# Performance work log

Hardware: AMD Instinct MI355X
Metric: run time of the kernel (lower is better)

The kernel has to match this reference:

```python
import jax, jax.numpy as jnp
import numpy as np

B, S, D, H = 4, 2048, 1024, 16
HD = D // H  # head_dim = 64


def setup_inputs() -> dict:
    key = jax.random.key(0)
    ks = jax.random.split(key, 10)
    scale = 1.0 / np.sqrt(D)
    x = jax.random.normal(ks[0], (B, S, D), dtype=jnp.float32)
    mask = jax.random.randint(ks[1], (B, S, S), 0, 2, dtype=jnp.int32)
    Wq = jax.random.normal(ks[2], (D, D), dtype=jnp.float32) * scale
    Wk = jax.random.normal(ks[3], (D, D), dtype=jnp.float32) * scale
    Wv = jax.random.normal(ks[4], (D, D), dtype=jnp.float32) * scale
    Wo = jax.random.normal(ks[5], (D, D), dtype=jnp.float32) * scale
    bq = jax.random.normal(ks[6], (D,), dtype=jnp.float32) * 0.01
    bk = jax.random.normal(ks[7], (D,), dtype=jnp.float32) * 0.01
    bv = jax.random.normal(ks[8], (D,), dtype=jnp.float32) * 0.01
    bo = jax.random.normal(ks[9], (D,), dtype=jnp.float32) * 0.01
    return {"x": x, "mask": mask, "Wq": Wq, "bq": bq, "Wk": Wk, "bk": bk,
            "Wv": Wv, "bv": bv, "Wo": Wo, "bo": bo}


def reference(x, mask, Wq, bq, Wk, bk, Wv, bv, Wo, bo):
    # QKV projections (nn.Linear: x @ W^T + b; W stored pre-transposed here as [D,D])
    q = x @ Wq + bq  # [B,S,D]
    k = x @ Wk + bk
    v = x @ Wv + bv
    # split heads -> [B,H,S,HD]
    def heads(t):
        return t.reshape(B, S, H, HD).transpose(0, 2, 1, 3)
    q, k, v = heads(q), heads(k), heads(v)
    scores = jnp.einsum('bhqd,bhkd->bhqk', q, k) / jnp.sqrt(jnp.float32(HD))
    # mask: [B,S,S] -> broadcast over heads; positions where mask==0 get -inf
    scores = jnp.where(mask[:, None, :, :] == 0, -jnp.inf, scores)
    attn = jax.nn.softmax(scores, axis=-1)
    attn = jnp.where(jnp.isnan(attn), 0.0, attn)  # nan_to_num(nan=0.0)
    out = jnp.einsum('bhqk,bhkd->bhqd', attn, v)  # [B,H,S,HD]
    out = out.transpose(0, 2, 1, 3).reshape(B, S, D)
    return out @ Wo + bo
```

## Files before the change

kernel.cpp:

```cpp
#include <hip/hip_runtime.h>
#include <hip/hip_bf16.h>
#include <stdint.h>

#define B_  4
#define S_  2048
#define D_  1024
#define H_  16
#define HD_ 64

typedef __attribute__((ext_vector_type(4))) float f32x4;
typedef __attribute__((ext_vector_type(8))) short bf16x8;

typedef const unsigned int __attribute__((address_space(1)))* gas_ptr;
typedef unsigned int __attribute__((address_space(3)))* las_ptr;

__device__ __forceinline__ void async16(const void* g, void* l) {
  __builtin_amdgcn_global_load_lds((gas_ptr)g, (las_ptr)l, 16, 0, 0);
}

__global__ __launch_bounds__(256) void cvt_x(const float* __restrict__ in,
                                             __hip_bfloat16* __restrict__ out,
                                             int n) {
  const int i = (blockIdx.x * blockDim.x + threadIdx.x) * 4;
  if (i >= n) return;
  const float4 v = *(const float4*)(in + i);
  union { ushort4 u; __hip_bfloat16 h[4]; } o;
  o.h[0] = (__hip_bfloat16)v.x;
  o.h[1] = (__hip_bfloat16)v.y;
  o.h[2] = (__hip_bfloat16)v.z;
  o.h[3] = (__hip_bfloat16)v.w;
  *(ushort4*)(out + i) = o.u;
}

__global__ __launch_bounds__(256) void expand_mask(const int* __restrict__ mk,
                                                   uint2* __restrict__ xm) {
  const unsigned j = blockIdx.x * 256 + threadIdx.x;
  const int mt = j & 3, quad = (j >> 2) & 3, kt = (j >> 4) & 31;
  const int q = (j >> 9) & 2047, b = j >> 20;
  const size_t row = (size_t)b * 2048 + q;
  const int key = kt * 64 + mt * 16 + quad * 4;
  const int4 m = *(const int4*)(mk + row * 2048 + key);
  uint2 o;
  o.x = (m.x ? 0xFFFFu : 0u) | (m.y ? 0xFFFF0000u : 0u);
  o.y = (m.z ? 0xFFFFu : 0u) | (m.w ? 0xFFFF0000u : 0u);
  xm[j] = o;
}

__global__ void transpose_w(const float* __restrict__ Wq,
                            const float* __restrict__ Wk,
                            const float* __restrict__ Wv,
                            const float* __restrict__ Wo,
                            __hip_bfloat16* __restrict__ Wt_qkv,
                            __hip_bfloat16* __restrict__ Wt_o) {
  __shared__ float t[32][33];
  const int z = blockIdx.z;
  const float* W = (z == 0) ? Wq : (z == 1) ? Wk : (z == 2) ? Wv : Wo;
  __hip_bfloat16* Wt = (z < 3) ? (Wt_qkv + (size_t)z * D_ * D_) : Wt_o;
  const int x = blockIdx.x * 32 + threadIdx.x;
  const int y = blockIdx.y * 32 + threadIdx.y;
  t[threadIdx.y][threadIdx.x] = W[(size_t)y * D_ + x];
  __syncthreads();
  const int xo = blockIdx.y * 32 + threadIdx.x;
  const int yo = blockIdx.x * 32 + threadIdx.y;
  Wt[(size_t)yo * D_ + xo] = (__hip_bfloat16)t[threadIdx.x][threadIdx.y];
}

__global__ __launch_bounds__(256) void gemm_qkv(
    const __hip_bfloat16* __restrict__ A,
    const __hip_bfloat16* __restrict__ Bt,
    const float* __restrict__ bq,
    const float* __restrict__ bk,
    const float* __restrict__ bv,
    __hip_bfloat16* __restrict__ QKo,
    __hip_bfloat16* __restrict__ Vt) {
  __shared__ __hip_bfloat16 sA[128 * 32];
  __shared__ __hip_bfloat16 sB[128 * 32];
  const int K = 1024;
  const int tid  = threadIdx.x;
  const int wave = tid >> 6;
  const int lane = tid & 63;
  const int quad = lane >> 4;
  const int l16  = lane & 15;
  const int wg  = blockIdx.x;
  const int swz = (wg & 7) * 192 + (wg >> 3);
  const int bm = (swz / 24) * 128;
  const int bn = (swz % 24) * 128;
  const int wm = (wave >> 1) * 64;
  const int wn = (wave & 1) * 64;

  const int r0 = wave * 2, r1 = wave * 2 + 1;
  const int lrow = lane >> 2;
  const int lcol = (lane & 3) * 8;

  const __hip_bfloat16* ga0 = A  + (size_t)(bm + r0 * 16 + lrow) * K + lcol;
  const __hip_bfloat16* ga1 = A  + (size_t)(bm + r1 * 16 + lrow) * K + lcol;
  const __hip_bfloat16* gb0 = Bt + (size_t)(bn + r0 * 16 + lrow) * K + lcol;
  const __hip_bfloat16* gb1 = Bt + (size_t)(bn + r1 * 16 + lrow) * K + lcol;
  char* la0 = (char*)sA + r0 * 1024;
  char* la1 = (char*)sA + r1 * 1024;
  char* lb0 = (char*)sB + r0 * 1024;
  char* lb1 = (char*)sB + r1 * 1024;

  const char* pa = (const char*)sA + (wm + l16) * 64 + quad * 16;
  const char* pb = (const char*)sB + (wn + l16) * 64 + quad * 16;

  f32x4 acc[4][4] = {};

  for (int k0 = 0; k0 < K; k0 += 32) {
    async16(ga0 + k0, la0);
    async16(ga1 + k0, la1);
    async16(gb0 + k0, lb0);
    async16(gb1 + k0, lb1);
    __syncthreads();
    bf16x8 af[4], bf[4];
#pragma unroll
    for (int mt = 0; mt < 4; ++mt) af[mt] = *(const bf16x8*)(pa + mt * 1024);
#pragma unroll
    for (int nt = 0; nt < 4; ++nt) bf[nt] = *(const bf16x8*)(pb + nt * 1024);
#pragma unroll
    for (int mt = 0; mt < 4; ++mt)
#pragma unroll
      for (int nt = 0; nt < 4; ++nt)
        acc[mt][nt] = __builtin_amdgcn_mfma_f32_16x16x32_bf16(af[mt], bf[nt], acc[mt][nt], 0, 0, 0);
    __syncthreads();
  }

#pragma unroll
  for (int mt = 0; mt < 4; ++mt) {
    const int row = bm + wm + mt * 16 + quad * 4;
#pragma unroll
    for (int nt = 0; nt < 4; ++nt) {
      const int col = bn + wn + nt * 16 + l16;
      f32x4 v = acc[mt][nt];
      if (col < 2048) {
        const float bias = (col < 1024) ? bq[col] : bk[col - 1024];
        const float sc = (col < 1024) ? 0.18033688011f : 1.0f;
#pragma unroll
        for (int r = 0; r < 4; ++r)
          QKo[(size_t)(row + r) * 2048 + col] = (__hip_bfloat16)((v[r] + bias) * sc);
      } else {
        const int cv = col - 2048;
        const float bias = bv[cv];
        const int hh = cv >> 6, d = cv & 63;
        const int bb = row >> 11, s0 = row & 2047;
        union { __hip_bfloat16 h[4]; unsigned long long u; } pk;
#pragma unroll
        for (int r = 0; r < 4; ++r) pk.h[r] = (__hip_bfloat16)(v[r] + bias);
        *(unsigned long long*)(Vt + ((size_t)(bb * 16 + hh) * 64 + d) * 2048 + s0) = pk.u;
      }
    }
  }
}

__global__ __launch_bounds__(256) void gemm_out(
    const __hip_bfloat16* __restrict__ A,
    const __hip_bfloat16* __restrict__ Bt,
    const float* __restrict__ b0,
    float* __restrict__ C,
    int N, int K) {
  __shared__ __hip_bfloat16 sA[128 * 32];
  __shared__ __hip_bfloat16 sB[128 * 32];
  const int tid  = threadIdx.x;
  const int wave = tid >> 6;
  const int lane = tid & 63;
  const int quad = lane >> 4;
  const int l16  = lane & 15;
  const int wg  = blockIdx.x;
  const int swz = (wg & 7) * 64 + (wg >> 3);
  const int bm = (swz >> 3) * 128;
  const int bn = (swz & 7) * 128;
  const int wm = (wave >> 1) * 64;
  const int wn = (wave & 1) * 64;

  const int r0 = wave * 2, r1 = wave * 2 + 1;
  const int lrow = lane >> 2;
  const int lcol = (lane & 3) * 8;

  const __hip_bfloat16* ga0 = A  + (size_t)(bm + r0 * 16 + lrow) * K + lcol;
  const __hip_bfloat16* ga1 = A  + (size_t)(bm + r1 * 16 + lrow) * K + lcol;
  const __hip_bfloat16* gb0 = Bt + (size_t)(bn + r0 * 16 + lrow) * K + lcol;
  const __hip_bfloat16* gb1 = Bt + (size_t)(bn + r1 * 16 + lrow) * K + lcol;
  char* la0 = (char*)sA + r0 * 1024;
  char* la1 = (char*)sA + r1 * 1024;
  char* lb0 = (char*)sB + r0 * 1024;
  char* lb1 = (char*)sB + r1 * 1024;

  const char* pa = (const char*)sA + (wm + l16) * 64 + quad * 16;
  const char* pb = (const char*)sB + (wn + l16) * 64 + quad * 16;

  f32x4 acc[4][4] = {};

  for (int k0 = 0; k0 < K; k0 += 32) {
    async16(ga0 + k0, la0);
    async16(ga1 + k0, la1);
    async16(gb0 + k0, lb0);
    async16(gb1 + k0, lb1);
    __syncthreads();
    bf16x8 af[4], bf[4];
#pragma unroll
    for (int mt = 0; mt < 4; ++mt) af[mt] = *(const bf16x8*)(pa + mt * 1024);
#pragma unroll
    for (int nt = 0; nt < 4; ++nt) bf[nt] = *(const bf16x8*)(pb + nt * 1024);
#pragma unroll
    for (int mt = 0; mt < 4; ++mt)
#pragma unroll
      for (int nt = 0; nt < 4; ++nt)
        acc[mt][nt] = __builtin_amdgcn_mfma_f32_16x16x32_bf16(af[mt], bf[nt], acc[mt][nt], 0, 0, 0);
    __syncthreads();
  }

#pragma unroll
  for (int mt = 0; mt < 4; ++mt) {
    const int row = bm + wm + mt * 16 + quad * 4;
#pragma unroll
    for (int nt = 0; nt < 4; ++nt) {
      const int col = bn + wn + nt * 16 + l16;
      const float bias = b0[col];
      f32x4 v = acc[mt][nt];
#pragma unroll
      for (int r = 0; r < 4; ++r)
        C[(size_t)(row + r) * N + col] = v[r] + bias;
    }
  }
}

__global__ __launch_bounds__(256, 4) void flash_attn(
    const __hip_bfloat16* __restrict__ QK,
    const __hip_bfloat16* __restrict__ Vt,
    const uint4* __restrict__ XM,
    __hip_bfloat16* __restrict__ O) {
  __shared__ __hip_bfloat16 sK[2][64 * 64];
  __shared__ __hip_bfloat16 sV[2][64 * 64];

  const int qt = blockIdx.x, h = blockIdx.y, b = blockIdx.z;
  const int tid = threadIdx.x;
  const int wave = tid >> 6, lane = tid & 63, quad = lane >> 4, l16 = lane & 15;
  const int qbase = qt * 128;
  const size_t brow = (size_t)b * S_;
  const int bh = b * H_ + h;

  bf16x8 qf[2][2];
#pragma unroll
  for (int g = 0; g < 2; ++g) {
    const __hip_bfloat16* qrow =
        QK + (brow + qbase + g * 64 + wave * 16 + l16) * 2048 + h * 64;
#pragma unroll
    for (int c = 0; c < 2; ++c)
      qf[g][c] = *(const bf16x8*)(qrow + c * 32 + quad * 8);
  }

  const int srow = lane >> 3;
  const int schk = (lane & 7) ^ srow;
  const __hip_bfloat16* gk0 =
      QK + (brow + wave * 16 + srow) * 2048 + 1024 + h * 64 + schk * 8;
  const __hip_bfloat16* gk1 = gk0 + (size_t)8 * 2048;
  const __hip_bfloat16* gv0 =
      Vt + ((size_t)bh * 64 + wave * 16 + srow) * 2048 + schk * 8;
  const __hip_bfloat16* gv1 = gv0 + (size_t)8 * 2048;
  char* const lK[2] = {(char*)&sK[0][0] + wave * 2048, (char*)&sK[1][0] + wave * 2048};
  char* const lV[2] = {(char*)&sV[0][0] + wave * 2048, (char*)&sV[1][0] + wave * 2048};

  const uint4* xpa = XM + ((brow + qbase + wave * 16 + l16) * 256 + quad * 2);
  const uint4* xpb = xpa + (size_t)64 * 256;

  const int xl = l16 & 7;
  const int koff0 = ((quad ^ xl) * 16);
  const int rowb = l16 * 128;

  const bf16x8 onesv = {(short)0x3F80, (short)0x3F80, (short)0x3F80, (short)0x3F80,
                        (short)0x3F80, (short)0x3F80, (short)0x3F80, (short)0x3F80};
  f32x4 lacc[2] = {};
  f32x4 oacc[2][4] = {};

  async16(gk0, lK[0]);
  async16(gk1, lK[0] + 1024);
  async16(gv0, lV[0]);
  async16(gv1, lV[0] + 1024);
  uint4 x0a = xpa[0], x1a = xpa[1], x0b = xpb[0], x1b = xpb[1];
  gk0 += (size_t)64 * 2048; gk1 += (size_t)64 * 2048;
  gv0 += 64; gv1 += 64;
  __syncthreads();

  const int NT = S_ / 64;
  for (int kt = 0; kt < NT; ++kt) {
    const int cur = kt & 1, nxt = cur ^ 1;

    if (kt + 1 < NT) {
      async16(gk0, lK[nxt]);
      async16(gk1, lK[nxt] + 1024);
      async16(gv0, lV[nxt]);
      async16(gv1, lV[nxt] + 1024);
      gk0 += (size_t)64 * 2048; gk1 += (size_t)64 * 2048;
      gv0 += 64; gv1 += 64;
    }
    const uint4 ca0 = x0a, ca1 = x1a, cb0 = x0b, cb1 = x1b;
    const int kn = (kt + 1 < NT) ? kt + 1 : kt;
    x0a = xpa[kn * 8]; x1a = xpa[kn * 8 + 1];
    x0b = xpb[kn * 8]; x1b = xpb[kn * 8 + 1];

    const char* bK = (const char*)&sK[cur][0] + rowb;
    unsigned pl[2][4][2];
#pragma unroll
    for (int mt = 0; mt < 4; ++mt) {
      const bf16x8 kf0 = *(const bf16x8*)(bK + mt * 2048 + koff0);
      const bf16x8 kf1 = *(const bf16x8*)(bK + mt * 2048 + (koff0 ^ 64));
      f32x4 a0 = {}, a1 = {};
      __builtin_amdgcn_s_setprio(1);
      a0 = __builtin_amdgcn_mfma_f32_16x16x32_bf16(kf0, qf[0][0], a0, 0, 0, 0);
      a0 = __builtin_amdgcn_mfma_f32_16x16x32_bf16(kf1, qf[0][1], a0, 0, 0, 0);
      a1 = __builtin_amdgcn_mfma_f32_16x16x32_bf16(kf0, qf[1][0], a1, 0, 0, 0);
      a1 = __builtin_amdgcn_mfma_f32_16x16x32_bf16(kf1, qf[1][1], a1, 0, 0, 0);
      __builtin_amdgcn_s_setprio(0);
#pragma unroll
      for (int g = 0; g < 2; ++g) {
        const uint4 cc = g ? ((mt < 2) ? cb0 : cb1) : ((mt < 2) ? ca0 : ca1);
        const unsigned w0 = (mt & 1) ? cc.z : cc.x;
        const unsigned w1 = (mt & 1) ? cc.w : cc.y;
        const f32x4 av = g ? a1 : a0;
        union { __hip_bfloat16 h[2]; unsigned u; } c0, c1;
        c0.h[0] = (__hip_bfloat16)__builtin_amdgcn_exp2f(av[0]);
        c0.h[1] = (__hip_bfloat16)__builtin_amdgcn_exp2f(av[1]);
        c1.h[0] = (__hip_bfloat16)__builtin_amdgcn_exp2f(av[2]);
        c1.h[1] = (__hip_bfloat16)__builtin_amdgcn_exp2f(av[3]);
        pl[g][mt][0] = c0.u & w0;
        pl[g][mt][1] = c1.u & w1;
      }
    }

    bf16x8 pf[2][2];
#pragma unroll
    for (int g = 0; g < 2; ++g)
#pragma unroll
      for (int c = 0; c < 2; ++c) {
        unsigned e0 = pl[g][2 * c][0], o0 = pl[g][2 * c + 1][0];
        unsigned e1 = pl[g][2 * c][1], o1 = pl[g][2 * c + 1][1];
        asm("v_permlane32_swap_b32 %0, %1" : "+v"(e0), "+v"(o0));
        asm("v_permlane16_swap_b32 %0, %1" : "+v"(e0), "+v"(o0));
        asm("v_permlane32_swap_b32 %0, %1" : "+v"(e1), "+v"(o1));
        asm("v_permlane16_swap_b32 %0, %1" : "+v"(e1), "+v"(o1));
        union { unsigned u[4]; bf16x8 v; } uu;
        uu.u[0] = e0; uu.u[1] = e1; uu.u[2] = o0; uu.u[3] = o1;
        pf[g][c] = uu.v;
      }

    const char* bV = (const char*)&sV[cur][0] + rowb;
    __builtin_amdgcn_s_setprio(1);
#pragma unroll
    for (int ht = 0; ht < 4; ++ht) {
      const bf16x8 vf0 = *(const bf16x8*)(bV + ht * 2048 + koff0);
      const bf16x8 vf1 = *(const bf16x8*)(bV + ht * 2048 + (koff0 ^ 64));
      oacc[0][ht] = __builtin_amdgcn_mfma_f32_16x16x32_bf16(vf0, pf[0][0], oacc[0][ht], 0, 0, 0);
      oacc[0][ht] = __builtin_amdgcn_mfma_f32_16x16x32_bf16(vf1, pf[0][1], oacc[0][ht], 0, 0, 0);
      oacc[1][ht] = __builtin_amdgcn_mfma_f32_16x16x32_bf16(vf0, pf[1][0], oacc[1][ht], 0, 0, 0);
      oacc[1][ht] = __builtin_amdgcn_mfma_f32_16x16x32_bf16(vf1, pf[1][1], oacc[1][ht], 0, 0, 0);
    }
    lacc[0] = __builtin_amdgcn_mfma_f32_16x16x32_bf16(onesv, pf[0][0], lacc[0], 0, 0, 0);
    lacc[0] = __builtin_amdgcn_mfma_f32_16x16x32_bf16(onesv, pf[0][1], lacc[0], 0, 0, 0);
    lacc[1] = __builtin_amdgcn_mfma_f32_16x16x32_bf16(onesv, pf[1][0], lacc[1], 0, 0, 0);
    lacc[1] = __builtin_amdgcn_mfma_f32_16x16x32_bf16(onesv, pf[1][1], lacc[1], 0, 0, 0);
    __builtin_amdgcn_s_setprio(0);

    __syncthreads();
  }

#pragma unroll
  for (int g = 0; g < 2; ++g) {
    const float l = lacc[g][0];
    const float inv = (l > 0.f) ? 1.f / l : 0.f;
    __hip_bfloat16* orow =
        O + (brow + qbase + g * 64 + wave * 16 + l16) * 1024 + h * 64;
#pragma unroll
    for (int ht = 0; ht < 4; ++ht) {
      union { __hip_bfloat16 h[4]; unsigned long long u; } ok_;
#pragma unroll
      for (int r = 0; r < 4; ++r) ok_.h[r] = (__hip_bfloat16)(oacc[g][ht][r] * inv);
      *(unsigned long long*)(orow + ht * 16 + quad * 4) = ok_.u;
    }
  }
}

extern "C" void kernel_launch(void* const* d_in, const int* in_sizes, int n_in,
                              void* d_out, int out_size, void* d_ws, size_t ws_size,
                              hipStream_t stream) {
  const float* x  = (const float*)d_in[0];
  const int*   mk = (const int*)d_in[1];
  const float* Wq = (const float*)d_in[2];
  const float* bq = (const float*)d_in[3];
  const float* Wk = (const float*)d_in[4];
  const float* bk = (const float*)d_in[5];
  const float* Wv = (const float*)d_in[6];
  const float* bv = (const float*)d_in[7];
  const float* Wo = (const float*)d_in[8];
  const float* bo = (const float*)d_in[9];
  float* out = (float*)d_out;

  __hip_bfloat16* X16    = (__hip_bfloat16*)d_ws;
  __hip_bfloat16* Wt_qkv = X16 + (size_t)B_ * S_ * D_;
  __hip_bfloat16* Wt_o   = Wt_qkv + (size_t)3 * D_ * D_;
  __hip_bfloat16* QK     = Wt_o + (size_t)D_ * D_;
  __hip_bfloat16* Vt     = QK + (size_t)B_ * S_ * 2 * D_;
  __hip_bfloat16* Obuf   = Vt + (size_t)B_ * H_ * HD_ * S_;
  unsigned* xmask = (unsigned*)(Obuf + (size_t)B_ * S_ * D_);

  const int nx = B_ * S_ * D_;
  cvt_x<<<dim3((nx / 4 + 255) / 256), 256, 0, stream>>>(x, X16, nx);
  transpose_w<<<dim3(32, 32, 4), dim3(32, 32), 0, stream>>>(Wq, Wk, Wv, Wo, Wt_qkv, Wt_o);
  expand_mask<<<dim3((int)((size_t)B_ * S_ * S_ / 4 / 256)), 256, 0, stream>>>(
      mk, (uint2*)xmask);
  gemm_qkv<<<dim3(24 * 64), 256, 0, stream>>>(
      X16, Wt_qkv, bq, bk, bv, QK, Vt);
  flash_attn<<<dim3(S_ / 128, H_, B_), 256, 0, stream>>>(
      QK, Vt, (const uint4*)xmask, Obuf);
  gemm_out<<<dim3(8 * 64), 256, 0, stream>>>(
      Obuf, Wt_o, bo, out, D_, D_);
}
```

Measured before the change: 360.2 us.

## Double GEMM K-tile to 64 with XOR-swizzled LDS layout in projection kernels

Both projection GEMMs now stage 128x64 bf16 tiles of A and B per iteration instead of 128x32. That halves the number of __syncthreads barriers and loop iterations over K. The LDS layout is XOR-swizzled on 16-byte chunks, on both the global_load_lds writes and the fragment reads, to avoid bank conflicts on the wider 128-byte rows. LDS use per block doubles to 32KB, which may reduce occupancy, and loads are still not overlapped with compute.

```diff
diff --git a/kernel.cpp b/kernel.cpp
--- a/kernel.cpp
+++ b/kernel.cpp
@@ -73,8 +73,8 @@
     const float* __restrict__ bv,
     __hip_bfloat16* __restrict__ QKo,
     __hip_bfloat16* __restrict__ Vt) {
-  __shared__ __hip_bfloat16 sA[128 * 32];
-  __shared__ __hip_bfloat16 sB[128 * 32];
+  __shared__ __hip_bfloat16 sA[128 * 64];
+  __shared__ __hip_bfloat16 sB[128 * 64];
   const int K = 1024;
   const int tid  = threadIdx.x;
   const int wave = tid >> 6;
@@ -88,40 +88,41 @@
   const int wm = (wave >> 1) * 64;
   const int wn = (wave & 1) * 64;
 
-  const int r0 = wave * 2, r1 = wave * 2 + 1;
-  const int lrow = lane >> 2;
-  const int lcol = (lane & 3) * 8;
-
-  const __hip_bfloat16* ga0 = A  + (size_t)(bm + r0 * 16 + lrow) * K + lcol;
-  const __hip_bfloat16* ga1 = A  + (size_t)(bm + r1 * 16 + lrow) * K + lcol;
-  const __hip_bfloat16* gb0 = Bt + (size_t)(bn + r0 * 16 + lrow) * K + lcol;
-  const __hip_bfloat16* gb1 = Bt + (size_t)(bn + r1 * 16 + lrow) * K + lcol;
-  char* la0 = (char*)sA + r0 * 1024;
-  char* la1 = (char*)sA + r1 * 1024;
-  char* lb0 = (char*)sB + r0 * 1024;
-  char* lb1 = (char*)sB + r1 * 1024;
-
-  const char* pa = (const char*)sA + (wm + l16) * 64 + quad * 16;
-  const char* pb = (const char*)sB + (wn + l16) * 64 + quad * 16;
+  const int srow = lane >> 3;
+  const int schk = (lane & 7) ^ srow;
+  const __hip_bfloat16* gA = A  + (size_t)(bm + wave * 32 + srow) * K + schk * 8;
+  const __hip_bfloat16* gB = Bt + (size_t)(bn + wave * 32 + srow) * K + schk * 8;
+  char* const lA = (char*)sA + wave * 32 * 128;
+  char* const lB = (char*)sB + wave * 32 * 128;
+
+  const int xl = l16 & 7;
+  const int koff = (quad ^ xl) * 16;
+  const char* pa = (const char*)sA + (wm + l16) * 128;
+  const char* pb = (const char*)sB + (wn + l16) * 128;
 
   f32x4 acc[4][4] = {};
 
-  for (int k0 = 0; k0 < K; k0 += 32) {
-    async16(ga0 + k0, la0);
-    async16(ga1 + k0, la1);
-    async16(gb0 + k0, lb0);
-    async16(gb1 + k0, lb1);
+  for (int k0 = 0; k0 < K; k0 += 64) {
+#pragma unroll
+    for (int t = 0; t < 4; ++t) {
+      async16(gA + (size_t)(t * 8) * K + k0, lA + t * 1024);
+      async16(gB + (size_t)(t * 8) * K + k0, lB + t * 1024);
+    }
     __syncthreads();
-    bf16x8 af[4], bf[4];
-#pragma unroll
-    for (int mt = 0; mt < 4; ++mt) af[mt] = *(const bf16x8*)(pa + mt * 1024);
-#pragma unroll
-    for (int nt = 0; nt < 4; ++nt) bf[nt] = *(const bf16x8*)(pb + nt * 1024);
-#pragma unroll
-    for (int mt = 0; mt < 4; ++mt)
-#pragma unroll
-      for (int nt = 0; nt < 4; ++nt)
-        acc[mt][nt] = __builtin_amdgcn_mfma_f32_16x16x32_bf16(af[mt], bf[nt], acc[mt][nt], 0, 0, 0);
+#pragma unroll
+    for (int c = 0; c < 2; ++c) {
+      const int off = koff ^ (c * 64);
+      bf16x8 af[4], bf[4];
+#pragma unroll
+      for (int mt = 0; mt < 4; ++mt) af[mt] = *(const bf16x8*)(pa + mt * 2048 + off);
+#pragma unroll
+      for (int nt = 0; nt < 4; ++nt) bf[nt] = *(const bf16x8*)(pb + nt * 2048 + off);
+#pragma unroll
+      for (int mt = 0; mt < 4; ++mt)
+#pragma unroll
+        for (int nt = 0; nt < 4; ++nt)
+          acc[mt][nt] = __builtin_amdgcn_mfma_f32_16x16x32_bf16(af[mt], bf[nt], acc[mt][nt], 0, 0, 0);
+    }
     __syncthreads();
   }
 
@@ -158,8 +159,8 @@
     const float* __restrict__ b0,
     float* __restrict__ C,
     int N, int K) {
-  __shared__ __hip_bfloat16 sA[128 * 32];
-  __shared__ __hip_bfloat16 sB[128 * 32];
+  __shared__ __hip_bfloat16 sA[128 * 64];
+  __shared__ __hip_bfloat16 sB[128 * 64];
   const int tid  = threadIdx.x;
   const int wave = tid >> 6;
   const int lane = tid & 63;
@@ -172,40 +173,41 @@
   const int wm = (wave >> 1) * 64;
   const int wn = (wave & 1) * 64;
 
-  const int r0 = wave * 2, r1 = wave * 2 + 1;
-  const int lrow = lane >> 2;
-  const int lcol = (lane & 3) * 8;
-
-  const __hip_bfloat16* ga0 = A  + (size_t)(bm + r0 * 16 + lrow) * K + lcol;
-  const __hip_bfloat16* ga1 = A  + (size_t)(bm + r1 * 16 + lrow) * K + lcol;
-  const __hip_bfloat16* gb0 = Bt + (size_t)(bn + r0 * 16 + lrow) * K + lcol;
-  const __hip_bfloat16* gb1 = Bt + (size_t)(bn + r1 * 16 + lrow) * K + lcol;
-  char* la0 = (char*)sA + r0 * 1024;
-  char* la1 = (char*)sA + r1 * 1024;
-  char* lb0 = (char*)sB + r0 * 1024;
-  char* lb1 = (char*)sB + r1 * 1024;
-
-  const char* pa = (const char*)sA + (wm + l16) * 64 + quad * 16;
-  const char* pb = (const char*)sB + (wn + l16) * 64 + quad * 16;
+  const int srow = lane >> 3;
+  const int schk = (lane & 7) ^ srow;
+  const __hip_bfloat16* gA = A  + (size_t)(bm + wave * 32 + srow) * K + schk * 8;
+  const __hip_bfloat16* gB = Bt + (size_t)(bn + wave * 32 + srow) * K + schk * 8;
+  char* const lA = (char*)sA + wave * 32 * 128;
+  char* const lB = (char*)sB + wave * 32 * 128;
+
+  const int xl = l16 & 7;
+  const int koff = (quad ^ xl) * 16;
+  const char* pa = (const char*)sA + (wm + l16) * 128;
+  const char* pb = (const char*)sB + (wn + l16) * 128;
 
   f32x4 acc[4][4] = {};
 
-  for (int k0 = 0; k0 < K; k0 += 32) {
-    async16(ga0 + k0, la0);
-    async16(ga1 + k0, la1);
-    async16(gb0 + k0, lb0);
-    async16(gb1 + k0, lb1);
+  for (int k0 = 0; k0 < K; k0 += 64) {
+#pragma unroll
+    for (int t = 0; t < 4; ++t) {
+      async16(gA + (size_t)(t * 8) * K + k0, lA + t * 1024);
+      async16(gB + (size_t)(t * 8) * K + k0, lB + t * 1024);
+    }
     __syncthreads();
-    bf16x8 af[4], bf[4];
-#pragma unroll
-    for (int mt = 0; mt < 4; ++mt) af[mt] = *(const bf16x8*)(pa + mt * 1024);
-#pragma unroll
-    for (int nt = 0; nt < 4; ++nt) bf[nt] = *(const bf16x8*)(pb + nt * 1024);
-#pragma unroll
-    for (int mt = 0; mt < 4; ++mt)
-#pragma unroll
-      for (int nt = 0; nt < 4; ++nt)
-        acc[mt][nt] = __builtin_amdgcn_mfma_f32_16x16x32_bf16(af[mt], bf[nt], acc[mt][nt], 0, 0, 0);
+#pragma unroll
+    for (int c = 0; c < 2; ++c) {
+      const int off = koff ^ (c * 64);
+      bf16x8 af[4], bf[4];
+#pragma unroll
+      for (int mt = 0; mt < 4; ++mt) af[mt] = *(const bf16x8*)(pa + mt * 2048 + off);
+#pragma unroll
+      for (int nt = 0; nt < 4; ++nt) bf[nt] = *(const bf16x8*)(pb + nt * 2048 + off);
+#pragma unroll
+      for (int mt = 0; mt < 4; ++mt)
+#pragma unroll
+        for (int nt = 0; nt < 4; ++nt)
+          acc[mt][nt] = __builtin_amdgcn_mfma_f32_16x16x32_bf16(af[mt], bf[nt], acc[mt][nt], 0, 0, 0);
+    }
     __syncthreads();
   }
 
```

Result: no change. 357.8 us (-0.7%).
